# Kernel optimization log

Measured on AMD Instinct MI355X. Metric: run time of the kernel, lower is better.

The kernel has to match this reference:

```python
import jax, jax.numpy as jnp
import numpy as np

B, Cin, Cout, H, W, K, S, P = 8, 128, 128, 64, 64, 3, 1, 1


def setup_inputs() -> dict:
    key = jax.random.key(0)
    k1, k2, k3 = jax.random.split(key, 3)
    x = jax.random.normal(k1, (B, Cin, H, W), jnp.float32)
    # offset-predicting conv weight (zero-init in the original; use small random for a nontrivial test)
    w_offset = jax.random.normal(k2, (2 * K * K, Cin, K, K), jnp.float32) * 0.01
    # deformable conv weight, uniform(-stdv, stdv) with stdv = 1/sqrt(Cin*K*K)
    stdv = 1.0 / np.sqrt(Cin * K * K)
    w = jax.random.uniform(k3, (Cout, Cin, K, K), jnp.float32, -stdv, stdv)
    return {"x": x, "w_offset": w_offset, "w": w}


def _conv2d(x, w, stride, pad):
    return jax.lax.conv_general_dilated(
        x, w, (stride, stride), [(pad, pad), (pad, pad)],
        dimension_numbers=("NCHW", "OIHW", "NCHW"))


def _deform_conv(x, offset, w, stride, pad):
    # x: [B,C,H,W]; offset: [B,2*K*K,Ho,Wo] as (dy,dx) pairs per kernel tap; w: [Cout,C,K,K]
    Bb, C, Hh, Ww = x.shape
    Co, _, Kk, _ = w.shape
    _, _, Ho, Wo = offset.shape
    KK = Kk * Kk
    off = offset.reshape(Bb, KK, 2, Ho, Wo)
    dy, dx = off[:, :, 0], off[:, :, 1]              # [B,KK,Ho,Wo]

    ky, kx = jnp.meshgrid(jnp.arange(Kk), jnp.arange(Kk), indexing="ij")
    ky = ky.reshape(KK).astype(x.dtype)
    kx = kx.reshape(KK).astype(x.dtype)
    oy = (jnp.arange(Ho) * stride - pad).astype(x.dtype)
    ox = (jnp.arange(Wo) * stride - pad).astype(x.dtype)

    # absolute sampling coordinates per kernel tap: [B,KK,Ho,Wo]
    py = oy[None, None, :, None] + ky[None, :, None, None] + dy
    px = ox[None, None, None, :] + kx[None, :, None, None] + dx

    y0 = jnp.floor(py)
    x0 = jnp.floor(px)
    ly = py - y0
    lx = px - x0
    y0i = y0.astype(jnp.int32)
    x0i = x0.astype(jnp.int32)

    xf = x.reshape(Bb, C, Hh * Ww)

    def gather(yi, xi):
        valid = (yi >= 0) & (yi < Hh) & (xi >= 0) & (xi < Ww)
        yc = jnp.clip(yi, 0, Hh - 1)
        xc = jnp.clip(xi, 0, Ww - 1)
        idx = (yc * Ww + xc).reshape(Bb, -1)          # [B, KK*Ho*Wo]
        v = jax.vmap(lambda xb, ib: xb[:, ib])(xf, idx)  # [B, C, KK*Ho*Wo]
        return v * valid.reshape(Bb, 1, -1).astype(x.dtype)

    v00 = gather(y0i, x0i)
    v01 = gather(y0i, x0i + 1)
    v10 = gather(y0i + 1, x0i)
    v11 = gather(y0i + 1, x0i + 1)

    wy = ly.reshape(Bb, 1, -1)
    wx = lx.reshape(Bb, 1, -1)
    sampled = (v00 * (1 - wy) * (1 - wx) + v01 * (1 - wy) * wx
               + v10 * wy * (1 - wx) + v11 * wy * wx)   # [B, C, KK*Ho*Wo]
    sampled = sampled.reshape(Bb, C, KK, Ho * Wo)

    out = jnp.einsum("bckl,ock->bol", sampled, w.reshape(Co, C, KK))
    return out.reshape(Bb, Co, Ho, Wo)


def reference(x, w_offset, w):
    offset = _conv2d(x, w_offset, S, P)   # [B, 2*K*K, Ho, Wo]
    return _deform_conv(x, offset, w, S, P)
```

## Files before the change

### kernel.cpp

```cpp
#include <hip/hip_runtime.h>
#include <hip/hip_bf16.h>
#include <math.h>


typedef short bf16x8 __attribute__((ext_vector_type(8)));
typedef float f32x4  __attribute__((ext_vector_type(4)));

__device__ __forceinline__ unsigned short f2bf(float f) {
    unsigned u = __float_as_uint(f);
    u += 0x7fffu + ((u >> 16) & 1u);
    return (unsigned short)(u >> 16);
}
__device__ __forceinline__ float bflo(unsigned u) { return __uint_as_float(u << 16); }
__device__ __forceinline__ float bfhi(unsigned u) { return __uint_as_float(u & 0xffff0000u); }

__global__ __launch_bounds__(256) void prep_weights(
    const float* __restrict__ w, const float* __restrict__ woff,
    unsigned short* __restrict__ wT, unsigned short* __restrict__ woffT) {
    int idx = blockIdx.x * 256 + threadIdx.x;
    if (idx < 147456) {
        int c  = idx & 127;
        int co = (idx >> 7) & 127;
        int kk = idx >> 14;
        wT[idx] = f2bf(w[co * 1152 + c * 9 + kk]);
    }
    if (idx < 36864) {
        int c  = idx & 127;
        int oc = (idx >> 7) & 31;
        int kk = idx >> 12;
        woffT[idx] = (oc < 18) ? f2bf(woff[oc * 1152 + c * 9 + kk]) : (unsigned short)0;
    }
}

__global__ __launch_bounds__(256) void transpose_nchw_nhwc(
    const float* __restrict__ x, unsigned* __restrict__ xT) {
    __shared__ float tile[128][65];
    int bh = blockIdx.x;
    int b = bh >> 6, h = bh & 63;
    const float* src = x + b * 524288 + h * 64;
    for (int idx = threadIdx.x; idx < 8192; idx += 256) {
        int c = idx >> 6, ww = idx & 63;
        tile[c][ww] = src[c * 4096 + ww];
    }
    __syncthreads();
    unsigned* dst = xT + (size_t)bh * 4096;
    for (int idx = threadIdx.x; idx < 4096; idx += 256) {
        int ww = idx >> 6, c2 = (idx & 63) * 2;
        unsigned lo = f2bf(tile[c2][ww]);
        unsigned hi = f2bf(tile[c2 + 1][ww]);
        dst[idx] = lo | (hi << 16);
    }
}

__global__ __launch_bounds__(256) void offset_mfma(
    const __hip_bfloat16* __restrict__ xT, const unsigned short* __restrict__ woffT,
    _Float16* __restrict__ offT) {
    int blk = blockIdx.x;
    int b = blk >> 6, ho = blk & 63;
    int t = threadIdx.x, l = t & 63, w = t >> 6;
    int lr = l & 15, lg = l >> 4;
    const char* xb = (const char*)xT + (size_t)b * 1048576;
    f32x4 acc[2] = {{0.f,0.f,0.f,0.f},{0.f,0.f,0.f,0.f}};

    for (int kk = 0; kk < 9; ++kk) {
        int y = ho + kk / 3 - 1;
        if ((unsigned)y >= 64u) continue;
        int xcol = w * 16 + lr + kk % 3 - 1;
        bool vx = (unsigned)xcol < 64u;
#pragma unroll
        for (int kg = 0; kg < 4; ++kg) {
            int c0 = kg * 32 + lg * 8;
            bf16x8 A = {};
            if (vx) A = *(const bf16x8*)(xb + ((y * 64 + xcol) * 128 + c0) * 2);
#pragma unroll
            for (int n = 0; n < 2; ++n) {
                bf16x8 Bf = *(const bf16x8*)(woffT + (kk * 32 + n * 16 + lr) * 128 + c0);
                acc[n] = __builtin_amdgcn_mfma_f32_16x16x32_bf16(A, Bf, acc[n], 0, 0, 0);
            }
        }
    }
    _Float16* orow = offT + (size_t)b * 4096 * 18;
    int posb = ho * 64 + w * 16 + lg * 4;
#pragma unroll
    for (int n = 0; n < 2; ++n) {
        int oc = n * 16 + lr;
        if (oc < 18) {
#pragma unroll
            for (int r = 0; r < 4; ++r)
                orow[(posb + r) * 18 + oc] = (_Float16)acc[n][r];
        }
    }
}

__global__ __launch_bounds__(512) void deform_mfma(
    const __hip_bfloat16* __restrict__ xT, const _Float16* __restrict__ offT,
    const unsigned short* __restrict__ wT, float* __restrict__ out) {
    __shared__ unsigned short s_tile[8192];
    __shared__ int4   s_pix[576];
    __shared__ float4 s_wt[576];

    int blk = blockIdx.x;
    int b = blk >> 6, ho = blk & 63;
    int t = threadIdx.x, l = t & 63, w = t >> 6;
    int lr = l & 15, lg = l >> 4;
    const char* xb = (const char*)xT + (size_t)b * 1048576;

    const unsigned* ou = (const unsigned*)offT;
    for (int e = t; e < 576; e += 512) {
        int pos = e & 63, kk = e >> 6;
        unsigned pr = ou[(size_t)(b * 4096 + ho * 64 + pos) * 9 + kk];
        union { unsigned u; _Float16 h[2]; } cv; cv.u = pr;
        float dy = (float)cv.h[0], dx = (float)cv.h[1];
        float py = (float)(ho + kk / 3 - 1) + dy;
        float px = (float)(pos + kk % 3 - 1) + dx;
        float y0f = floorf(py), x0f = floorf(px);
        float ly = py - y0f, lx = px - x0f;
        int y0 = (int)y0f, x0 = (int)x0f;
        int y1 = y0 + 1, x1 = x0 + 1;
        float my0 = ((unsigned)y0 < 64u) ? 1.f : 0.f;
        float my1 = ((unsigned)y1 < 64u) ? 1.f : 0.f;
        float mx0 = ((unsigned)x0 < 64u) ? 1.f : 0.f;
        float mx1 = ((unsigned)x1 < 64u) ? 1.f : 0.f;
        int y0c = min(max(y0, 0), 63), y1c = min(max(y1, 0), 63);
        int x0c = min(max(x0, 0), 63), x1c = min(max(x1, 0), 63);
        s_pix[e] = make_int4((y0c * 64 + x0c) * 256, (y0c * 64 + x1c) * 256,
                             (y1c * 64 + x0c) * 256, (y1c * 64 + x1c) * 256);
        s_wt[e] = make_float4((1.f - ly) * (1.f - lx) * my0 * mx0,
                              (1.f - ly) * lx * my0 * mx1,
                              ly * (1.f - lx) * my1 * mx0,
                              ly * lx * my1 * mx1);
    }
    __syncthreads();

    f32x4 acc[4] = {{0.f,0.f,0.f,0.f},{0.f,0.f,0.f,0.f},{0.f,0.f,0.f,0.f},{0.f,0.f,0.f,0.f}};
    char* tp = (char*)s_tile;
    int pg = t >> 5;
    int cq = t & 31;
    int cb = w * 16;

    for (int kk = 0; kk < 9; ++kk) {
#pragma unroll
        for (int i = 0; i < 4; ++i) {
            int pos = pg + i * 16;
            int e = kk * 64 + pos;
            int4 pix = s_pix[e];
            float4 wt = s_wt[e];
            uint2 u00 = *(const uint2*)(xb + pix.x + cq * 8);
            uint2 u01 = *(const uint2*)(xb + pix.y + cq * 8);
            uint2 u10 = *(const uint2*)(xb + pix.z + cq * 8);
            uint2 u11 = *(const uint2*)(xb + pix.w + cq * 8);
            float r0 = wt.x * bflo(u00.x) + wt.y * bflo(u01.x) + wt.z * bflo(u10.x) + wt.w * bflo(u11.x);
            float r1 = wt.x * bfhi(u00.x) + wt.y * bfhi(u01.x) + wt.z * bfhi(u10.x) + wt.w * bfhi(u11.x);
            float r2 = wt.x * bflo(u00.y) + wt.y * bflo(u01.y) + wt.z * bflo(u10.y) + wt.w * bflo(u11.y);
            float r3 = wt.x * bfhi(u00.y) + wt.y * bfhi(u01.y) + wt.z * bfhi(u10.y) + wt.w * bfhi(u11.y);
            uint2 o;
            o.x = (unsigned)f2bf(r0) | ((unsigned)f2bf(r1) << 16);
            o.y = (unsigned)f2bf(r2) | ((unsigned)f2bf(r3) << 16);
            *(uint2*)(tp + pos * 256 + (((cq >> 1) ^ (pos & 7)) << 4) + (cq & 1) * 8) = o;
        }
        bf16x8 Af[4];
        {
            const unsigned short* wr = wT + ((kk * 128 + cb + lr) << 7) + lg * 8;
#pragma unroll
            for (int kg = 0; kg < 4; ++kg)
                Af[kg] = *(const bf16x8*)(wr + kg * 32);
        }
        __syncthreads();
#pragma unroll
        for (int kg = 0; kg < 4; ++kg) {
            int slot = kg * 4 + lg;
#pragma unroll
            for (int n = 0; n < 4; ++n) {
                int row = n * 16 + lr;
                bf16x8 Bf = *(const bf16x8*)(tp + row * 256 + ((slot ^ (row & 7)) << 4));
                acc[n] = __builtin_amdgcn_mfma_f32_16x16x32_bf16(Af[kg], Bf, acc[n], 0, 0, 0);
            }
        }
        __syncthreads();
    }

    float* ob = out + ((size_t)(b * 128 + cb + lg * 4)) * 4096 + ho * 64;
#pragma unroll
    for (int n = 0; n < 4; ++n) {
#pragma unroll
        for (int r = 0; r < 4; ++r)
            ob[r * 4096 + n * 16 + lr] = acc[n][r];
    }
}

extern "C" void kernel_launch(void* const* d_in, const int* in_sizes, int n_in,
                              void* d_out, int out_size, void* d_ws, size_t ws_size,
                              hipStream_t stream) {
    const float* x    = (const float*)d_in[0];
    const float* woff = (const float*)d_in[1];
    const float* w    = (const float*)d_in[2];
    float* out = (float*)d_out;

    unsigned short* wT    = (unsigned short*)d_ws;
    unsigned short* woffT = (unsigned short*)((char*)d_ws + 294912);
    _Float16*       offT  = (_Float16*)((char*)d_ws + 368640);
    __hip_bfloat16* xT    = (__hip_bfloat16*)((char*)d_ws + 1548288);

    prep_weights<<<576, 256, 0, stream>>>(w, woff, wT, woffT);
    transpose_nchw_nhwc<<<512, 256, 0, stream>>>(x, (unsigned*)xT);
    offset_mfma<<<512, 256, 0, stream>>>(xT, woffT, offT);
    deform_mfma<<<512, 512, 0, stream>>>(xT, offT, wT, out);
}
```

Before: 140.2 us.

## Fuse offset conv into deformable conv kernel and double-buffer sampled tile

The offset-predicting convolution is computed inside the deformable conv block and kept in shared memory in fp32, which removes a separate kernel launch and the fp16 offset round-trip through global memory. The bilinear gather loop is also software-pipelined: loads for the next kernel tap are issued before the MFMA work on the current tap, with a double-buffered LDS tile. This costs extra shared memory and registers per block, which may lower occupancy, and the offset conv work is spread over 8 waves per block.

```diff
diff --git a/kernel.cpp b/kernel.cpp
--- a/kernel.cpp
+++ b/kernel.cpp
@@ -52,65 +52,51 @@
     }
 }
 
-__global__ __launch_bounds__(256) void offset_mfma(
-    const __hip_bfloat16* __restrict__ xT, const unsigned short* __restrict__ woffT,
-    _Float16* __restrict__ offT) {
+__global__ __launch_bounds__(512, 4) void deform_fused(
+    const __hip_bfloat16* __restrict__ xT,
+    const unsigned short* __restrict__ wT,
+    const unsigned short* __restrict__ woffT,
+    float* __restrict__ out) {
+    __shared__ unsigned short s_tile[2][8192];
+    __shared__ float  s_off[18][64];
+    __shared__ int4   s_pix[576];
+    __shared__ float4 s_wt[576];
+
     int blk = blockIdx.x;
     int b = blk >> 6, ho = blk & 63;
     int t = threadIdx.x, l = t & 63, w = t >> 6;
     int lr = l & 15, lg = l >> 4;
     const char* xb = (const char*)xT + (size_t)b * 1048576;
-    f32x4 acc[2] = {{0.f,0.f,0.f,0.f},{0.f,0.f,0.f,0.f}};
-
-    for (int kk = 0; kk < 9; ++kk) {
-        int y = ho + kk / 3 - 1;
-        if ((unsigned)y >= 64u) continue;
-        int xcol = w * 16 + lr + kk % 3 - 1;
-        bool vx = (unsigned)xcol < 64u;
-#pragma unroll
-        for (int kg = 0; kg < 4; ++kg) {
-            int c0 = kg * 32 + lg * 8;
-            bf16x8 A = {};
-            if (vx) A = *(const bf16x8*)(xb + ((y * 64 + xcol) * 128 + c0) * 2);
-#pragma unroll
-            for (int n = 0; n < 2; ++n) {
-                bf16x8 Bf = *(const bf16x8*)(woffT + (kk * 32 + n * 16 + lr) * 128 + c0);
-                acc[n] = __builtin_amdgcn_mfma_f32_16x16x32_bf16(A, Bf, acc[n], 0, 0, 0);
+
+    {
+        int m4 = w >> 1, n2 = w & 1;
+        f32x4 oacc = {0.f, 0.f, 0.f, 0.f};
+        for (int kk = 0; kk < 9; ++kk) {
+            int y = ho + kk / 3 - 1;
+            if ((unsigned)y >= 64u) continue;
+            int xcol = m4 * 16 + lr + kk % 3 - 1;
+            bool vx = (unsigned)xcol < 64u;
+            const unsigned short* wo = woffT + (kk * 32 + n2 * 16 + lr) * 128 + lg * 8;
+#pragma unroll
+            for (int kg = 0; kg < 4; ++kg) {
+                bf16x8 A = {};
+                if (vx) A = *(const bf16x8*)(xb + ((y * 64 + xcol) * 128 + kg * 32 + lg * 8) * 2);
+                bf16x8 Bf = *(const bf16x8*)(wo + kg * 32);
+                oacc = __builtin_amdgcn_mfma_f32_16x16x32_bf16(A, Bf, oacc, 0, 0, 0);
             }
         }
-    }
-    _Float16* orow = offT + (size_t)b * 4096 * 18;
-    int posb = ho * 64 + w * 16 + lg * 4;
-#pragma unroll
-    for (int n = 0; n < 2; ++n) {
-        int oc = n * 16 + lr;
+        int oc = n2 * 16 + lr;
         if (oc < 18) {
 #pragma unroll
             for (int r = 0; r < 4; ++r)
-                orow[(posb + r) * 18 + oc] = (_Float16)acc[n][r];
-        }
-    }
-}
-
-__global__ __launch_bounds__(512) void deform_mfma(
-    const __hip_bfloat16* __restrict__ xT, const _Float16* __restrict__ offT,
-    const unsigned short* __restrict__ wT, float* __restrict__ out) {
-    __shared__ unsigned short s_tile[8192];
-    __shared__ int4   s_pix[576];
-    __shared__ float4 s_wt[576];
-
-    int blk = blockIdx.x;
-    int b = blk >> 6, ho = blk & 63;
-    int t = threadIdx.x, l = t & 63, w = t >> 6;
-    int lr = l & 15, lg = l >> 4;
-    const char* xb = (const char*)xT + (size_t)b * 1048576;
-
-    const unsigned* ou = (const unsigned*)offT;
+                s_off[oc][m4 * 16 + lg * 4 + r] = oacc[r];
+        }
+    }
+    __syncthreads();
+
     for (int e = t; e < 576; e += 512) {
         int pos = e & 63, kk = e >> 6;
-        unsigned pr = ou[(size_t)(b * 4096 + ho * 64 + pos) * 9 + kk];
-        union { unsigned u; _Float16 h[2]; } cv; cv.u = pr;
-        float dy = (float)cv.h[0], dx = (float)cv.h[1];
+        float dy = s_off[2 * kk][pos], dx = s_off[2 * kk + 1][pos];
         float py = (float)(ho + kk / 3 - 1) + dy;
         float px = (float)(pos + kk % 3 - 1) + dx;
         float y0f = floorf(py), x0f = floorf(px);
@@ -132,50 +118,66 @@
     }
     __syncthreads();
 
-    f32x4 acc[4] = {{0.f,0.f,0.f,0.f},{0.f,0.f,0.f,0.f},{0.f,0.f,0.f,0.f},{0.f,0.f,0.f,0.f}};
-    char* tp = (char*)s_tile;
     int pg = t >> 5;
     int cq = t & 31;
     int cb = w * 16;
-
-    for (int kk = 0; kk < 9; ++kk) {
+    int coff = cq * 8;
+    f32x4 acc[4] = {{0.f,0.f,0.f,0.f},{0.f,0.f,0.f,0.f},{0.f,0.f,0.f,0.f},{0.f,0.f,0.f,0.f}};
+    uint2 u[4][4];
+
+    auto issue = [&](int kk) {
 #pragma unroll
         for (int i = 0; i < 4; ++i) {
             int pos = pg + i * 16;
-            int e = kk * 64 + pos;
-            int4 pix = s_pix[e];
-            float4 wt = s_wt[e];
-            uint2 u00 = *(const uint2*)(xb + pix.x + cq * 8);
-            uint2 u01 = *(const uint2*)(xb + pix.y + cq * 8);
-            uint2 u10 = *(const uint2*)(xb + pix.z + cq * 8);
-            uint2 u11 = *(const uint2*)(xb + pix.w + cq * 8);
-            float r0 = wt.x * bflo(u00.x) + wt.y * bflo(u01.x) + wt.z * bflo(u10.x) + wt.w * bflo(u11.x);
-            float r1 = wt.x * bfhi(u00.x) + wt.y * bfhi(u01.x) + wt.z * bfhi(u10.x) + wt.w * bfhi(u11.x);
-            float r2 = wt.x * bflo(u00.y) + wt.y * bflo(u01.y) + wt.z * bflo(u10.y) + wt.w * bflo(u11.y);
-            float r3 = wt.x * bfhi(u00.y) + wt.y * bfhi(u01.y) + wt.z * bfhi(u10.y) + wt.w * bfhi(u11.y);
+            int4 pix = s_pix[kk * 64 + pos];
+            u[i][0] = *(const uint2*)(xb + pix.x + coff);
+            u[i][1] = *(const uint2*)(xb + pix.y + coff);
+            u[i][2] = *(const uint2*)(xb + pix.z + coff);
+            u[i][3] = *(const uint2*)(xb + pix.w + coff);
+        }
+    };
+    auto process = [&](int kk, int buf) {
+        char* tp = (char*)s_tile[buf];
+#pragma unroll
+        for (int i = 0; i < 4; ++i) {
+            int pos = pg + i * 16;
+            float4 wt = s_wt[kk * 64 + pos];
+            float r0 = wt.x * bflo(u[i][0].x) + wt.y * bflo(u[i][1].x) + wt.z * bflo(u[i][2].x) + wt.w * bflo(u[i][3].x);
+            float r1 = wt.x * bfhi(u[i][0].x) + wt.y * bfhi(u[i][1].x) + wt.z * bfhi(u[i][2].x) + wt.w * bfhi(u[i][3].x);
+            float r2 = wt.x * bflo(u[i][0].y) + wt.y * bflo(u[i][1].y) + wt.z * bflo(u[i][2].y) + wt.w * bflo(u[i][3].y);
+            float r3 = wt.x * bfhi(u[i][0].y) + wt.y * bfhi(u[i][1].y) + wt.z * bfhi(u[i][2].y) + wt.w * bfhi(u[i][3].y);
             uint2 o;
             o.x = (unsigned)f2bf(r0) | ((unsigned)f2bf(r1) << 16);
             o.y = (unsigned)f2bf(r2) | ((unsigned)f2bf(r3) << 16);
             *(uint2*)(tp + pos * 256 + (((cq >> 1) ^ (pos & 7)) << 4) + (cq & 1) * 8) = o;
         }
-        bf16x8 Af[4];
+    };
+
+    issue(0);
+    process(0, 0);
+    __syncthreads();
+
+    for (int kk = 0; kk < 9; ++kk) {
+        if (kk < 8) issue(kk + 1);
         {
             const unsigned short* wr = wT + ((kk * 128 + cb + lr) << 7) + lg * 8;
+            bf16x8 Af[4];
 #pragma unroll
             for (int kg = 0; kg < 4; ++kg)
                 Af[kg] = *(const bf16x8*)(wr + kg * 32);
-        }
-        __syncthreads();
-#pragma unroll
-        for (int kg = 0; kg < 4; ++kg) {
-            int slot = kg * 4 + lg;
-#pragma unroll
-            for (int n = 0; n < 4; ++n) {
-                int row = n * 16 + lr;
-                bf16x8 Bf = *(const bf16x8*)(tp + row * 256 + ((slot ^ (row & 7)) << 4));
-                acc[n] = __builtin_amdgcn_mfma_f32_16x16x32_bf16(Af[kg], Bf, acc[n], 0, 0, 0);
+            char* rp = (char*)s_tile[kk & 1];
+#pragma unroll
+            for (int kg = 0; kg < 4; ++kg) {
+                int slot = kg * 4 + lg;
+#pragma unroll
+                for (int n = 0; n < 4; ++n) {
+                    int row = n * 16 + lr;
+                    bf16x8 Bf = *(const bf16x8*)(rp + row * 256 + ((slot ^ (row & 7)) << 4));
+                    acc[n] = __builtin_amdgcn_mfma_f32_16x16x32_bf16(Af[kg], Bf, acc[n], 0, 0, 0);
+                }
             }
         }
+        if (kk < 8) process(kk + 1, (kk + 1) & 1);
         __syncthreads();
     }
 
@@ -198,11 +200,9 @@
 
     unsigned short* wT    = (unsigned short*)d_ws;
     unsigned short* woffT = (unsigned short*)((char*)d_ws + 294912);
-    _Float16*       offT  = (_Float16*)((char*)d_ws + 368640);
-    __hip_bfloat16* xT    = (__hip_bfloat16*)((char*)d_ws + 1548288);
+    __hip_bfloat16* xT    = (__hip_bfloat16*)((char*)d_ws + 368640);
 
     prep_weights<<<576, 256, 0, stream>>>(w, woff, wT, woffT);
     transpose_nchw_nhwc<<<512, 256, 0, stream>>>(x, (unsigned*)xT);
-    offset_mfma<<<512, 256, 0, stream>>>(xT, woffT, offT);
-    deform_mfma<<<512, 512, 0, stream>>>(xT, offT, wT, out);
-}
+    deform_fused<<<512, 512, 0, stream>>>(xT, wT, woffT, out);
+}
```

After: 149.2 us. 1.06x slower.
